# Kernel optimization log

Measured on AMD Instinct MI355X. Metric: run time of the kernel, lower is better.

The kernel has to match this reference:

```python
import jax, jax.numpy as jnp
import numpy as np

INF = 1e5
EPS = 1e-8
B, NRES, NRIG = 1, 448, 512
C_S, C_Z, C_H, H, PQ, PV = 384, 128, 16, 12, 4, 8


def _quat_to_rot(q):
    q = q / jnp.linalg.norm(q, axis=-1, keepdims=True)
    w, x, y, z = q[..., 0], q[..., 1], q[..., 2], q[..., 3]
    return jnp.stack([
        jnp.stack([1 - 2 * (y * y + z * z), 2 * (x * y - w * z), 2 * (x * z + w * y)], -1),
        jnp.stack([2 * (x * y + w * z), 1 - 2 * (x * x + z * z), 2 * (y * z - w * x)], -1),
        jnp.stack([2 * (x * z - w * y), 2 * (y * z + w * x), 1 - 2 * (x * x + y * y)], -1),
    ], -2)


def setup_inputs() -> dict:
    key = jax.random.key(0)
    ks = jax.random.split(key, 16)
    lin = lambda k, i, o: (jax.random.normal(k, (i, o), jnp.float32) / np.sqrt(i))
    hc = H * C_H
    return dict(
        s=jax.random.normal(ks[0], (B, NRIG, C_S), jnp.float32),
        z=jax.random.normal(ks[1], (B, NRES, NRES, C_Z), jnp.float32),
        rot=_quat_to_rot(jax.random.normal(ks[2], (B, NRIG, 4), jnp.float32)),
        trans=jax.random.normal(ks[3], (B, NRIG, 3), jnp.float32) * 10.0,
        mask=jnp.ones((B, NRIG), jnp.float32),
        rigid_to_res_idx=jax.random.randint(ks[4], (B, NRIG), 0, NRES),
        w_q=lin(ks[5], C_S, hc), b_q=jnp.zeros((hc,), jnp.float32),
        w_kv=lin(ks[6], C_S, 2 * hc), b_kv=jnp.zeros((2 * hc,), jnp.float32),
        w_qp=lin(ks[7], C_S, H * PQ * 3), b_qp=jnp.zeros((H * PQ * 3,), jnp.float32),
        w_kvp=lin(ks[8], C_S, H * (PQ + PV) * 3), b_kvp=jnp.zeros((H * (PQ + PV) * 3,), jnp.float32),
        w_b=lin(ks[9], C_Z, H), b_b=jnp.zeros((H,), jnp.float32),
        w_dz=lin(ks[10], C_Z, C_Z // 4), b_dz=jnp.zeros((C_Z // 4,), jnp.float32),
        head_weights=jnp.full((H,), 0.5413, jnp.float32),  # softplus^-1(1)
        w_out=lin(ks[11], H * (C_Z // 4 + C_H + PV * 4), C_S),
        b_out=jnp.zeros((C_S,), jnp.float32),
    )


def _fwd(s, z, rot, trans, mask, rigid_to_res_idx,
         w_q, b_q, w_kv, b_kv, w_qp, b_qp, w_kvp, b_kvp,
         w_b, b_b, w_dz, b_dz, head_weights, w_out, b_out):
    Bd, nr, _ = s.shape
    nres = z.shape[-2]
    h = w_b.shape[-1]
    ch = w_q.shape[-1] // h
    pq = w_qp.shape[-1] // (3 * h)
    pkv = w_kvp.shape[-1] // (3 * h)
    pv = pkv - pq

    q = (s @ w_q + b_q).reshape(Bd, nr, h, ch)
    kv = (s @ w_kv + b_kv).reshape(Bd, nr, h, 2 * ch)
    k, v = kv[..., :ch], kv[..., ch:]

    def to_pts(flat):
        # flat: [B,nr,3*D] laid out as 3 coordinate chunks -> global-frame pts [B,nr,D,3]
        D = flat.shape[-1] // 3
        p = jnp.moveaxis(flat.reshape(Bd, nr, 3, D), -2, -1)
        return jnp.einsum('bnij,bndj->bndi', rot, p) + trans[:, :, None, :]

    q_pts = to_pts(s @ w_qp + b_qp).reshape(Bd, nr, h, pq, 3)
    kv_pts = to_pts(s @ w_kvp + b_kvp).reshape(Bd, nr, h, pkv, 3)
    k_pts, v_pts = kv_pts[..., :pq, :], kv_pts[..., pq:, :]

    # pair bias gathered rigid->res on both axes
    bi = jnp.arange(Bd)[:, None, None]
    b_pair = z @ w_b + b_b  # [B,Nres,Nres,H]
    b_bcast = b_pair[bi, rigid_to_res_idx[:, :, None], rigid_to_res_idx[:, None, :]]  # [B,nr,nr,H]

    a = jnp.einsum('bihc,bjhc->bhij', q, k) * np.sqrt(1.0 / (3 * ch))
    a = a + np.sqrt(1.0 / 3) * jnp.moveaxis(b_bcast, -1, -3)

    # squared-distance point attention
    diff = q_pts[:, :, None] - k_pts[:, None]  # [B,nr,nr,h,pq,3]
    sq = jnp.sum(diff * diff, -1)              # [B,nr,nr,h,pq]
    hw = jax.nn.softplus(head_weights) * np.sqrt(1.0 / (3 * (pq * 9.0 / 2)))
    pt_att = -0.5 * jnp.sum(sq * hw[:, None], -1)  # [B,nr,nr,h]
    a = a + jnp.moveaxis(pt_att, -1, -3)

    sq_mask = INF * (mask[:, :, None] * mask[:, None, :] - 1.0)
    a = jax.nn.softmax(a + sq_mask[:, None], axis=-1)  # [B,h,nr,nr]

    o = jnp.einsum('bhij,bjhc->bihc', a, v).reshape(Bd, nr, h * ch)

    o_pt_g = jnp.einsum('bhij,bjhpx->bihpx', a, v_pts)  # [B,nr,h,pv,3]
    o_pt = jnp.einsum('bnji,bnhpj->bnhpi', rot, o_pt_g - trans[:, :, None, None, :])  # invert_apply
    o_pt_norm = jnp.sqrt(jnp.sum(o_pt * o_pt, -1) + EPS).reshape(Bd, nr, h * pv)
    o_pt = o_pt.reshape(Bd, nr, h * pv, 3)

    pair_z = z @ w_dz + b_dz  # [B,Nres,Nres,cz4]
    pz_rig = pair_z[jnp.arange(Bd)[:, None], rigid_to_res_idx]  # [B,nr,Nres,cz4]
    # faithful to the torch scatter_add_: the index varies over the QUERY rigid i
    # (constant over keys j), so row i's full softmax mass lands in column res(i).
    onehot = jax.nn.one_hot(rigid_to_res_idx, nres, dtype=a.dtype)  # [B,nr,Nres]
    a_agg = a.sum(-1)[..., None] * onehot[:, None]  # [B,h,nr,Nres]
    o_pair = jnp.einsum('bhin,bind->bihd', a_agg, pz_rig).reshape(Bd, nr, -1)

    feats = jnp.concatenate([o, o_pt[..., 0], o_pt[..., 1], o_pt[..., 2], o_pt_norm, o_pair], -1)
    return feats @ w_out + b_out


def reference(s, z, rot, trans, mask, rigid_to_res_idx, w_q, b_q, w_kv, b_kv, w_qp, b_qp, w_kvp, b_kvp, w_b, b_b, w_dz, b_dz, head_weights, w_out, b_out):
    return _fwd(s, z, rot, trans, mask, rigid_to_res_idx, w_q, b_q, w_kv, b_kv, w_qp, b_qp, w_kvp, b_kvp, w_b, b_b, w_dz, b_dz, head_weights, w_out, b_out)
```

## Files before the change

### kernel.cpp

```cpp
#include <hip/hip_runtime.h>
#include <hip/hip_bf16.h>
#include <math.h>

constexpr int NRIG = 512;
constexpr int NRES = 448;
constexpr int CS   = 384;
constexpr int CZ   = 128;
constexpr int CH   = 16;
constexpr int NH   = 12;
constexpr int PQ   = 4;
constexpr int PV   = 8;
constexpr int HC   = NH * CH;
constexpr float INF_ = 100000.0f;

constexpr size_t OFF_Q   = 0;
constexpr size_t OFF_K   = OFF_Q   + (size_t)NH*NRIG*16;
constexpr size_t OFF_QP  = OFF_K   + (size_t)NH*NRIG*16;
constexpr size_t OFF_KP  = OFF_QP  + (size_t)NH*NRIG*12;
constexpr size_t OFF_VT  = OFF_KP  + (size_t)NH*NRIG*12;
constexpr size_t OFF_PZ  = OFF_VT  + (size_t)NH*40*NRIG;
constexpr size_t OFF_O   = OFF_PZ  + (size_t)NRIG*32;
constexpr size_t OFF_OPT = OFF_O   + (size_t)NRIG*HC;
constexpr size_t OFF_RS  = OFF_OPT + (size_t)NRIG*NH*PV*3;
constexpr size_t OFF_B   = OFF_RS  + (size_t)NRIG*NH;
constexpr size_t OFF_RAW = OFF_B;
constexpr size_t OFF_F   = OFF_B;

__global__ __launch_bounds__(256) void proj_gemm_kernel(
    const float* __restrict__ s,
    const float* __restrict__ wq,  const float* __restrict__ bq,
    const float* __restrict__ wkv, const float* __restrict__ bkv,
    const float* __restrict__ wqp, const float* __restrict__ bqp,
    const float* __restrict__ wkvp,const float* __restrict__ bkvp,
    float* __restrict__ ws)
{
    constexpr int BM=64, BN=32, BK=32, LDA=68;
    __shared__ float sA[BK][LDA];
    __shared__ float sB[BK][BN];
    const int m0 = blockIdx.x * BM;
    const int c0 = blockIdx.y * BN;
    const int t  = threadIdx.x;
    const int tx = t & 15, ty = t >> 4;

    float acc[4][2] = {};

    for (int kt = 0; kt < CS/BK; ++kt) {
        const int k0 = kt*BK;
        #pragma unroll
        for (int r = 0; r < 2; ++r) {
            int qd = r*256 + t;
            int m = qd >> 3, kq = (qd & 7) << 2;
            float4 f = *(const float4*)(s + (size_t)(m0+m)*CS + k0 + kq);
            sA[kq+0][m] = f.x; sA[kq+1][m] = f.y;
            sA[kq+2][m] = f.z; sA[kq+3][m] = f.w;
        }
        {
            int kk = t >> 3, c4 = (t & 7) << 2;
            int c = c0 + c4;
            const float* wp; int ld, co;
            if (c < 192)      { wp = wq;   ld = 192; co = c;     }
            else if (c < 576) { wp = wkv;  ld = 384; co = c-192; }
            else if (c < 720) { wp = wqp;  ld = 144; co = c-576; }
            else              { wp = wkvp; ld = 432; co = c-720; }
            float4 f = *(const float4*)(wp + (size_t)(k0+kk)*ld + co);
            *(float4*)&sB[kk][c4] = f;
        }
        __syncthreads();
        #pragma unroll
        for (int kk = 0; kk < BK; ++kk) {
            float4 a = *(const float4*)&sA[kk][ty*4];
            float2 b = *(const float2*)&sB[kk][tx*2];
            acc[0][0] += a.x*b.x; acc[0][1] += a.x*b.y;
            acc[1][0] += a.y*b.x; acc[1][1] += a.y*b.y;
            acc[2][0] += a.z*b.x; acc[2][1] += a.z*b.y;
            acc[3][0] += a.w*b.x; acc[3][1] += a.w*b.y;
        }
        __syncthreads();
    }

    float* qw  = ws + OFF_Q;  float* kw = ws + OFF_K;  float* vt = ws + OFF_VT;
    float* raw = ws + OFF_RAW;
    #pragma unroll
    for (int i = 0; i < 4; ++i)
        #pragma unroll
        for (int j = 0; j < 2; ++j) {
            int n = m0 + ty*4 + i;
            int c = c0 + tx*2 + j;
            if (c < 192) {
                int hh = c >> 4, cc = c & 15;
                qw[((size_t)hh*NRIG + n)*16 + cc] = acc[i][j] + bq[c];
            } else if (c < 576) {
                int e = c-192; float val = acc[i][j] + bkv[e];
                int hh = e >> 5, sub = e & 31;
                if (sub < CH) kw[((size_t)hh*NRIG + n)*16 + sub] = val;
                else          vt[((size_t)hh*40 + (sub-CH))*NRIG + n] = val;
            } else {
                int e = c-576;
                float bb_ = (c < 720) ? bqp[e] : bkvp[c-720];
                raw[(size_t)n*576 + e] = acc[i][j] + bb_;
            }
        }
}

__global__ __launch_bounds__(256) void rotate_kernel(
    const float* __restrict__ rot, const float* __restrict__ trans,
    float* __restrict__ ws)
{
    const int gid = blockIdx.x*256 + threadIdx.x;
    const int n = gid / 192, d = gid % 192;
    const float* raw = ws + OFF_RAW + (size_t)n*576;
    float px, py, pzz;
    if (d < 48) { px = raw[d];      py = raw[48+d];       pzz = raw[96+d]; }
    else { int dd = d-48; px = raw[144+dd]; py = raw[288+dd]; pzz = raw[432+dd]; }
    const float* R = rot   + (size_t)n*9;
    const float* T = trans + (size_t)n*3;
    float gx = R[0]*px + R[1]*py + R[2]*pzz + T[0];
    float gy = R[3]*px + R[4]*py + R[5]*pzz + T[1];
    float gz = R[6]*px + R[7]*py + R[8]*pzz + T[2];
    if (d < 48) {
        int hh = d >> 2, pp = d & 3;
        float* dst = ws + OFF_QP + ((size_t)hh*NRIG + n)*12 + pp*3;
        dst[0]=gx; dst[1]=gy; dst[2]=gz;
    } else {
        int dd = d-48; int hh = dd/12, pp = dd%12;
        if (pp < PQ) {
            float* dst = ws + OFF_KP + ((size_t)hh*NRIG + n)*12 + pp*3;
            dst[0]=gx; dst[1]=gy; dst[2]=gz;
        } else {
            float* vt = ws + OFF_VT + ((size_t)hh*40 + 16 + (pp-PQ)*3)*NRIG + n;
            vt[0*NRIG]=gx; vt[1*NRIG]=gy; vt[2*NRIG]=gz;
        }
    }
}

__global__ __launch_bounds__(256) void bpair_kernel(
    const float* __restrict__ z, const int* __restrict__ ridx,
    const float* __restrict__ wb, const float* __restrict__ bb,
    const float* __restrict__ wdz, const float* __restrict__ bdz,
    float* __restrict__ ws)
{
    __shared__ float4 sWb[CZ*3];
    __shared__ float sZd[CZ];
    const int t = threadIdx.x;
    const int i = blockIdx.x;
    const int ri = ridx[i];
    for (int e = t; e < CZ*3; e += 256) sWb[e] = ((const float4*)wb)[e];
    if (t < CZ) sZd[t] = z[((size_t)ri*NRES + ri)*CZ + t];
    __syncthreads();

    const int j0  = t, j1 = t + 256;
    const int rj0 = ridx[j0], rj1 = ridx[j1];
    const float4* zr0 = (const float4*)(z + ((size_t)ri*NRES + rj0)*CZ);
    const float4* zr1 = (const float4*)(z + ((size_t)ri*NRES + rj1)*CZ);

    float a0[12], a1[12];
    #pragma unroll
    for (int hh=0; hh<12; ++hh) { a0[hh]=0.f; a1[hh]=0.f; }

    #pragma unroll 4
    for (int c4 = 0; c4 < 32; ++c4) {
        float4 z0 = zr0[c4], z1 = zr1[c4];
        #pragma unroll
        for (int e = 0; e < 4; ++e) {
            const int c = (c4<<2) + e;
            float wv[12];
            *(float4*)&wv[0] = sWb[c*3+0];
            *(float4*)&wv[4] = sWb[c*3+1];
            *(float4*)&wv[8] = sWb[c*3+2];
            const float zv0 = (&z0.x)[e];
            const float zv1 = (&z1.x)[e];
            #pragma unroll
            for (int hh=0; hh<12; ++hh) { a0[hh] += zv0*wv[hh]; a1[hh] += zv1*wv[hh]; }
        }
    }
    const float SC = 0.57735026918962584f;
    float* bbc = ws + OFF_B;
    #pragma unroll
    for (int hh = 0; hh < 12; ++hh) {
        float bias = bb[hh];
        bbc[((size_t)hh*NRIG + i)*NRIG + j0] = (a0[hh]+bias)*SC;
        bbc[((size_t)hh*NRIG + i)*NRIG + j1] = (a1[hh]+bias)*SC;
    }
    if (t < 32) {
        float acc = 0.f;
        for (int c = 0; c < CZ; ++c) acc += sZd[c] * wdz[(size_t)c*32 + t];
        (ws + OFF_PZ)[(size_t)i*32 + t] = acc + bdz[t];
    }
}

__global__ __launch_bounds__(256) void attn_kernel(
    const float* __restrict__ hw_in, const float* __restrict__ mask,
    float* __restrict__ ws)
{
    constexpr int TI = 4;
    const int h    = blockIdx.x;
    const int i0   = blockIdx.y * TI;
    const int t    = threadIdx.x;
    const int lane = t & 63, wid = t >> 6;

    __shared__ float sQ[TI][16];
    __shared__ float sQP[TI][12];
    __shared__ float sE[TI][512];
    __shared__ float redM[TI][4], redS[TI][4];
    __shared__ float sMi[TI];
    __shared__ float sP[TI][16][44];

    const float* qw  = ws + OFF_Q  + (size_t)h*NRIG*16;
    const float* kw  = ws + OFF_K  + (size_t)h*NRIG*16;
    const float* qpw = ws + OFF_QP + (size_t)h*NRIG*12;
    const float* kpw = ws + OFF_KP + (size_t)h*NRIG*12;
    const float* vt  = ws + OFF_VT + (size_t)h*40*NRIG;
    const float* bbc = ws + OFF_B  + (size_t)h*NRIG*NRIG;

    for (int e = t; e < TI*16; e += 256) sQ[e/16][e%16]  = qw[(size_t)(i0+e/16)*16 + (e%16)];
    for (int e = t; e < TI*12; e += 256) sQP[e/12][e%12] = qpw[(size_t)(i0+e/12)*12 + (e%12)];
    if (t < TI) sMi[t] = mask[i0+t];
    __syncthreads();

    const float hwv = -0.5f * log1pf(__expf(hw_in[h])) * 0.13608276348795434f;
    const float QKS = 0.14433756729740643f;

    float lg[2][TI];
    float lmax[TI] = {-1e30f,-1e30f,-1e30f,-1e30f};
    #pragma unroll
    for (int jj = 0; jj < 2; ++jj) {
        int j = t + jj*256;
        float kk[16], kpv[12];
        const float4* kr = (const float4*)(kw + (size_t)j*16);
        *(float4*)&kk[0]=kr[0]; *(float4*)&kk[4]=kr[1]; *(float4*)&kk[8]=kr[2]; *(float4*)&kk[12]=kr[3];
        const float4* kpr = (const float4*)(kpw + (size_t)j*12);
        *(float4*)&kpv[0]=kpr[0]; *(float4*)&kpv[4]=kpr[1]; *(float4*)&kpv[8]=kpr[2];
        float mj = mask[j];
        #pragma unroll
        for (int qq = 0; qq < TI; ++qq) {
            float dot = 0.f;
            #pragma unroll
            for (int c = 0; c < 16; ++c) dot += sQ[qq][c]*kk[c];
            float sq = 0.f;
            #pragma unroll
            for (int e = 0; e < 12; ++e) { float d = sQP[qq][e]-kpv[e]; sq += d*d; }
            float bv = bbc[(size_t)(i0+qq)*NRIG + j];
            float lgt = dot*QKS + bv + hwv*sq + INF_*(sMi[qq]*mj - 1.0f);
            lg[jj][qq] = lgt;
            lmax[qq] = fmaxf(lmax[qq], lgt);
        }
    }
    #pragma unroll
    for (int sft = 1; sft < 64; sft <<= 1)
        #pragma unroll
        for (int qq=0;qq<TI;++qq) lmax[qq] = fmaxf(lmax[qq], __shfl_xor(lmax[qq], sft));
    if (lane == 0) { for (int qq=0;qq<TI;++qq) redM[qq][wid] = lmax[qq]; }
    __syncthreads();
    float M[TI], psum[TI];
    #pragma unroll
    for (int qq=0;qq<TI;++qq) {
        M[qq] = fmaxf(fmaxf(redM[qq][0],redM[qq][1]),fmaxf(redM[qq][2],redM[qq][3]));
        psum[qq]=0.f;
    }
    #pragma unroll
    for (int jj = 0; jj < 2; ++jj) {
        int j = t + jj*256;
        #pragma unroll
        for (int qq=0;qq<TI;++qq) {
            float e = __expf(lg[jj][qq] - M[qq]);
            sE[qq][j] = e;
            psum[qq] += e;
        }
    }
    #pragma unroll
    for (int sft = 1; sft < 64; sft <<= 1)
        #pragma unroll
        for (int qq=0;qq<TI;++qq) psum[qq] += __shfl_xor(psum[qq], sft);
    if (lane == 0) { for (int qq=0;qq<TI;++qq) redS[qq][wid] = psum[qq]; }
    __syncthreads();

    {
        const int c0 = wid*10;
        float acc[10][TI];
        #pragma unroll
        for (int ci=0;ci<10;++ci)
            #pragma unroll
            for (int qq=0;qq<TI;++qq) acc[ci][qq]=0.f;

        #pragma unroll
        for (int m = 0; m < 8; ++m) {
            const int j = lane + 64*m;
            float ev[TI];
            #pragma unroll
            for (int qq=0;qq<TI;++qq) ev[qq] = sE[qq][j];
            #pragma unroll
            for (int ci = 0; ci < 10; ++ci) {
                float vv = vt[(size_t)(c0+ci)*NRIG + j];
                #pragma unroll
                for (int qq=0;qq<TI;++qq) acc[ci][qq] += ev[qq]*vv;
            }
        }
        #pragma unroll
        for (int ci=0;ci<10;++ci)
            #pragma unroll
            for (int qq=0;qq<TI;++qq) {
                acc[ci][qq] += __shfl_xor(acc[ci][qq], 1);
                acc[ci][qq] += __shfl_xor(acc[ci][qq], 2);
            }
        if ((lane & 3) == 0) {
            const int g = lane >> 2;
            #pragma unroll
            for (int qq=0;qq<TI;++qq)
                #pragma unroll
                for (int ci=0;ci<10;++ci)
                    sP[qq][g][c0+ci] = acc[ci][qq];
        }
    }
    __syncthreads();

    if (t < TI*41) {
        const int qq = t / 41, c = t % 41;
        const int n = i0 + qq;
        float S = redS[qq][0]+redS[qq][1]+redS[qq][2]+redS[qq][3];
        float Sinv = 1.0f / S;
        if (c == 40) {
            (ws + OFF_RS)[(size_t)n*NH + h] = S * Sinv;
        } else {
            float acc = 0.f;
            #pragma unroll
            for (int g = 0; g < 16; ++g) acc += sP[qq][g][c];
            acc *= Sinv;
            if (c < 16) (ws + OFF_O  )[((size_t)n*NH + h)*CH + c]      = acc;
            else        (ws + OFF_OPT)[((size_t)n*NH + h)*24 + (c-16)] = acc;
        }
    }
}

__global__ __launch_bounds__(256) void feats_kernel(
    const float* __restrict__ rot, const float* __restrict__ trans,
    float* __restrict__ ws)
{
    constexpr int TI = 4;
    const int i0 = blockIdx.x*TI;
    const int t  = threadIdx.x;
    float* F = ws + OFF_F;
    const float* o_ws = ws + OFF_O;  const float* optg = ws + OFF_OPT;
    const float* rs   = ws + OFF_RS; const float* pz   = ws + OFF_PZ;

    for (int e = t; e < TI*HC; e += 256) {
        int qq = e/HC, c = e%HC;
        F[(size_t)(i0+qq)*960 + c] = o_ws[(size_t)(i0+qq)*HC + c];
    }
    for (int e = t; e < TI*96; e += 256) {
        int qq = e/96, hp = e%96; int n = i0+qq;
        const float* g = optg + ((size_t)n*NH + hp/PV)*24 + (hp%PV)*3;
        float gx = g[0]-trans[n*3+0], gy = g[1]-trans[n*3+1], gz = g[2]-trans[n*3+2];
        const float* R = rot + (size_t)n*9;
        float lx = R[0]*gx + R[3]*gy + R[6]*gz;
        float ly = R[1]*gx + R[4]*gy + R[7]*gz;
        float lz = R[2]*gx + R[5]*gy + R[8]*gz;
        float* Fr = F + (size_t)n*960;
        Fr[192+hp] = lx; Fr[288+hp] = ly; Fr[384+hp] = lz;
        Fr[480+hp] = sqrtf(lx*lx+ly*ly+lz*lz + 1e-8f);
    }
    for (int e = t; e < TI*384; e += 256) {
        int qq = e/384, hd = e%384; int n = i0+qq;
        F[(size_t)n*960 + 576 + hd] = rs[(size_t)n*NH + hd/32] * pz[(size_t)n*32 + (hd%32)];
    }
}

__global__ __launch_bounds__(256) void out_gemm_kernel(
    const float* __restrict__ w_out, const float* __restrict__ b_out,
    const float* __restrict__ ws, float* __restrict__ out)
{
    constexpr int BM=64, BN=32, BK=32, LDA=68;
    __shared__ float sA[BK][LDA];
    __shared__ float sB[BK][BN];
    const float* F = ws + OFF_F;
    const int m0 = blockIdx.x * BM;
    const int c0 = blockIdx.y * BN;
    const int t  = threadIdx.x;
    const int tx = t & 15, ty = t >> 4;

    float acc[4][2] = {};

    for (int kt = 0; kt < 960/BK; ++kt) {
        const int k0 = kt*BK;
        #pragma unroll
        for (int r = 0; r < 2; ++r) {
            int qd = r*256 + t;
            int m = qd >> 3, kq = (qd & 7) << 2;
            float4 f = *(const float4*)(F + (size_t)(m0+m)*960 + k0 + kq);
            sA[kq+0][m] = f.x; sA[kq+1][m] = f.y;
            sA[kq+2][m] = f.z; sA[kq+3][m] = f.w;
        }
        {
            int kk = t >> 3, c4 = (t & 7) << 2;
            float4 f = *(const float4*)(w_out + (size_t)(k0+kk)*CS + c0 + c4);
            *(float4*)&sB[kk][c4] = f;
        }
        __syncthreads();
        #pragma unroll
        for (int kk = 0; kk < BK; ++kk) {
            float4 a = *(const float4*)&sA[kk][ty*4];
            float2 b = *(const float2*)&sB[kk][tx*2];
            acc[0][0] += a.x*b.x; acc[0][1] += a.x*b.y;
            acc[1][0] += a.y*b.x; acc[1][1] += a.y*b.y;
            acc[2][0] += a.z*b.x; acc[2][1] += a.z*b.y;
            acc[3][0] += a.w*b.x; acc[3][1] += a.w*b.y;
        }
        __syncthreads();
    }

    #pragma unroll
    for (int i = 0; i < 4; ++i)
        #pragma unroll
        for (int j = 0; j < 2; ++j) {
            int n = m0 + ty*4 + i;
            int c = c0 + tx*2 + j;
            out[(size_t)n*CS + c] = acc[i][j] + b_out[c];
        }
}

extern "C" void kernel_launch(void* const* d_in, const int* in_sizes, int n_in,
                              void* d_out, int out_size, void* d_ws, size_t ws_size,
                              hipStream_t stream)
{
    const float* s     = (const float*)d_in[0];
    const float* z     = (const float*)d_in[1];
    const float* rot   = (const float*)d_in[2];
    const float* trans = (const float*)d_in[3];
    const float* mask  = (const float*)d_in[4];
    const int*   ridx  = (const int*)  d_in[5];
    const float* wq    = (const float*)d_in[6];
    const float* bq    = (const float*)d_in[7];
    const float* wkv   = (const float*)d_in[8];
    const float* bkv   = (const float*)d_in[9];
    const float* wqp   = (const float*)d_in[10];
    const float* bqp   = (const float*)d_in[11];
    const float* wkvp  = (const float*)d_in[12];
    const float* bkvp  = (const float*)d_in[13];
    const float* wb    = (const float*)d_in[14];
    const float* bb    = (const float*)d_in[15];
    const float* wdz   = (const float*)d_in[16];
    const float* bdz   = (const float*)d_in[17];
    const float* hw    = (const float*)d_in[18];
    const float* wout  = (const float*)d_in[19];
    const float* bout  = (const float*)d_in[20];
    float* ws  = (float*)d_ws;
    float* out = (float*)d_out;

    hipLaunchKernelGGL(proj_gemm_kernel, dim3(NRIG/64, 1152/32), dim3(256), 0, stream,
        s, wq,bq, wkv,bkv, wqp,bqp, wkvp,bkvp, ws);
    hipLaunchKernelGGL(rotate_kernel, dim3(NRIG*192/256), dim3(256), 0, stream,
        rot, trans, ws);
    hipLaunchKernelGGL(bpair_kernel, dim3(NRIG), dim3(256), 0, stream,
        z, ridx, wb, bb, wdz, bdz, ws);
    hipLaunchKernelGGL(attn_kernel, dim3(NH, NRIG/4), dim3(256), 0, stream,
        hw, mask, ws);
    hipLaunchKernelGGL(feats_kernel, dim3(NRIG/4), dim3(256), 0, stream,
        rot, trans, ws);
    hipLaunchKernelGGL(out_gemm_kernel, dim3(NRIG/64, CS/32), dim3(256), 0, stream,
        wout, bout, ws, out);
}
```

Measured before the change: 122.0 us.

## Compute pair bias over all residue pairs, gather in attention, transpose K layouts

The pair-bias projection now runs once over every residue pair of z, writing a compact [Nres*Nres,12] table. The attention kernel gathers from this table by rigid-to-residue index instead of reading a precomputed per-head [H,Nrig,Nrig] bias. The diagonal z row used for pair_z moves into the feats kernel. K and K-point tensors are stored transposed so per-key loads coalesce, and the output GEMM uses smaller tiles to launch more blocks. The full z is now read densely (about 100MB) rather than through gathered rows, and the attention bias loads become scattered gathers.

```diff
diff --git a/kernel.cpp b/kernel.cpp
--- a/kernel.cpp
+++ b/kernel.cpp
@@ -11,20 +11,20 @@
 constexpr int PQ   = 4;
 constexpr int PV   = 8;
 constexpr int HC   = NH * CH;
+constexpr int NPAIR = NRES*NRES;
 constexpr float INF_ = 100000.0f;
 
 constexpr size_t OFF_Q   = 0;
-constexpr size_t OFF_K   = OFF_Q   + (size_t)NH*NRIG*16;
-constexpr size_t OFF_QP  = OFF_K   + (size_t)NH*NRIG*16;
-constexpr size_t OFF_KP  = OFF_QP  + (size_t)NH*NRIG*12;
-constexpr size_t OFF_VT  = OFF_KP  + (size_t)NH*NRIG*12;
-constexpr size_t OFF_PZ  = OFF_VT  + (size_t)NH*40*NRIG;
-constexpr size_t OFF_O   = OFF_PZ  + (size_t)NRIG*32;
+constexpr size_t OFF_KT  = OFF_Q   + (size_t)NH*NRIG*16;
+constexpr size_t OFF_QP  = OFF_KT  + (size_t)NH*16*NRIG;
+constexpr size_t OFF_KPT = OFF_QP  + (size_t)NH*NRIG*12;
+constexpr size_t OFF_VT  = OFF_KPT + (size_t)NH*12*NRIG;
+constexpr size_t OFF_O   = OFF_VT  + (size_t)NH*40*NRIG;
 constexpr size_t OFF_OPT = OFF_O   + (size_t)NRIG*HC;
 constexpr size_t OFF_RS  = OFF_OPT + (size_t)NRIG*NH*PV*3;
-constexpr size_t OFF_B   = OFF_RS  + (size_t)NRIG*NH;
-constexpr size_t OFF_RAW = OFF_B;
-constexpr size_t OFF_F   = OFF_B;
+constexpr size_t OFF_BP  = OFF_RS  + (size_t)NRIG*NH;
+constexpr size_t OFF_RAW = OFF_BP;
+constexpr size_t OFF_F   = OFF_BP;
 
 __global__ __launch_bounds__(256) void proj_gemm_kernel(
     const float* __restrict__ s,
@@ -78,7 +78,7 @@
         __syncthreads();
     }
 
-    float* qw  = ws + OFF_Q;  float* kw = ws + OFF_K;  float* vt = ws + OFF_VT;
+    float* qw  = ws + OFF_Q;  float* ktw = ws + OFF_KT;  float* vt = ws + OFF_VT;
     float* raw = ws + OFF_RAW;
     #pragma unroll
     for (int i = 0; i < 4; ++i)
@@ -92,8 +92,8 @@
             } else if (c < 576) {
                 int e = c-192; float val = acc[i][j] + bkv[e];
                 int hh = e >> 5, sub = e & 31;
-                if (sub < CH) kw[((size_t)hh*NRIG + n)*16 + sub] = val;
-                else          vt[((size_t)hh*40 + (sub-CH))*NRIG + n] = val;
+                if (sub < CH) ktw[((size_t)hh*16 + sub)*NRIG + n] = val;
+                else          vt [((size_t)hh*40 + (sub-CH))*NRIG + n] = val;
             } else {
                 int e = c-576;
                 float bb_ = (c < 720) ? bqp[e] : bkvp[c-720];
@@ -124,8 +124,10 @@
     } else {
         int dd = d-48; int hh = dd/12, pp = dd%12;
         if (pp < PQ) {
-            float* dst = ws + OFF_KP + ((size_t)hh*NRIG + n)*12 + pp*3;
-            dst[0]=gx; dst[1]=gy; dst[2]=gz;
+            float* kpt = ws + OFF_KPT + (size_t)hh*12*NRIG;
+            kpt[(size_t)(pp*3+0)*NRIG + n] = gx;
+            kpt[(size_t)(pp*3+1)*NRIG + n] = gy;
+            kpt[(size_t)(pp*3+2)*NRIG + n] = gz;
         } else {
             float* vt = ws + OFF_VT + ((size_t)hh*40 + 16 + (pp-PQ)*3)*NRIG + n;
             vt[0*NRIG]=gx; vt[1*NRIG]=gy; vt[2*NRIG]=gz;
@@ -133,63 +135,45 @@
     }
 }
 
-__global__ __launch_bounds__(256) void bpair_kernel(
-    const float* __restrict__ z, const int* __restrict__ ridx,
+__global__ __launch_bounds__(256) void zwb_kernel(
+    const float* __restrict__ z,
     const float* __restrict__ wb, const float* __restrict__ bb,
-    const float* __restrict__ wdz, const float* __restrict__ bdz,
     float* __restrict__ ws)
 {
-    __shared__ float4 sWb[CZ*3];
-    __shared__ float sZd[CZ];
+    constexpr int BR = 64, LDZ = 132;
+    __shared__ float sZ[BR][LDZ];
+    __shared__ float sW[CZ*12];
     const int t = threadIdx.x;
-    const int i = blockIdx.x;
-    const int ri = ridx[i];
-    for (int e = t; e < CZ*3; e += 256) sWb[e] = ((const float4*)wb)[e];
-    if (t < CZ) sZd[t] = z[((size_t)ri*NRES + ri)*CZ + t];
-    __syncthreads();
-
-    const int j0  = t, j1 = t + 256;
-    const int rj0 = ridx[j0], rj1 = ridx[j1];
-    const float4* zr0 = (const float4*)(z + ((size_t)ri*NRES + rj0)*CZ);
-    const float4* zr1 = (const float4*)(z + ((size_t)ri*NRES + rj1)*CZ);
-
-    float a0[12], a1[12];
-    #pragma unroll
-    for (int hh=0; hh<12; ++hh) { a0[hh]=0.f; a1[hh]=0.f; }
-
-    #pragma unroll 4
-    for (int c4 = 0; c4 < 32; ++c4) {
-        float4 z0 = zr0[c4], z1 = zr1[c4];
-        #pragma unroll
-        for (int e = 0; e < 4; ++e) {
-            const int c = (c4<<2) + e;
-            float wv[12];
-            *(float4*)&wv[0] = sWb[c*3+0];
-            *(float4*)&wv[4] = sWb[c*3+1];
-            *(float4*)&wv[8] = sWb[c*3+2];
-            const float zv0 = (&z0.x)[e];
-            const float zv1 = (&z1.x)[e];
-            #pragma unroll
-            for (int hh=0; hh<12; ++hh) { a0[hh] += zv0*wv[hh]; a1[hh] += zv1*wv[hh]; }
-        }
+    const size_t r0 = (size_t)blockIdx.x * BR;
+
+    for (int e = t; e < CZ*12; e += 256) sW[e] = wb[e];
+    #pragma unroll
+    for (int p = 0; p < 8; ++p) {
+        int q = p*256 + t;
+        int r = q >> 5, c4 = (q & 31) << 2;
+        float4 f = *(const float4*)(z + (r0 + r)*CZ + c4);
+        *(float4*)&sZ[r][c4] = f;
+    }
+    __syncthreads();
+
+    const int r = t >> 2, g = t & 3;
+    float a0=0.f, a1=0.f, a2=0.f;
+    #pragma unroll 8
+    for (int c = 0; c < CZ; ++c) {
+        float zv = sZ[r][c];
+        const float* w = &sW[c*12 + g*3];
+        a0 += zv*w[0]; a1 += zv*w[1]; a2 += zv*w[2];
     }
     const float SC = 0.57735026918962584f;
-    float* bbc = ws + OFF_B;
-    #pragma unroll
-    for (int hh = 0; hh < 12; ++hh) {
-        float bias = bb[hh];
-        bbc[((size_t)hh*NRIG + i)*NRIG + j0] = (a0[hh]+bias)*SC;
-        bbc[((size_t)hh*NRIG + i)*NRIG + j1] = (a1[hh]+bias)*SC;
-    }
-    if (t < 32) {
-        float acc = 0.f;
-        for (int c = 0; c < CZ; ++c) acc += sZd[c] * wdz[(size_t)c*32 + t];
-        (ws + OFF_PZ)[(size_t)i*32 + t] = acc + bdz[t];
-    }
+    float* bp = ws + OFF_BP + (r0 + r)*12 + g*3;
+    bp[0] = (a0 + bb[g*3+0])*SC;
+    bp[1] = (a1 + bb[g*3+1])*SC;
+    bp[2] = (a2 + bb[g*3+2])*SC;
 }
 
 __global__ __launch_bounds__(256) void attn_kernel(
     const float* __restrict__ hw_in, const float* __restrict__ mask,
+    const int* __restrict__ ridx,
     float* __restrict__ ws)
 {
     constexpr int TI = 4;
@@ -203,18 +187,19 @@
     __shared__ float sE[TI][512];
     __shared__ float redM[TI][4], redS[TI][4];
     __shared__ float sMi[TI];
+    __shared__ int   sRi[TI];
     __shared__ float sP[TI][16][44];
 
-    const float* qw  = ws + OFF_Q  + (size_t)h*NRIG*16;
-    const float* kw  = ws + OFF_K  + (size_t)h*NRIG*16;
-    const float* qpw = ws + OFF_QP + (size_t)h*NRIG*12;
-    const float* kpw = ws + OFF_KP + (size_t)h*NRIG*12;
-    const float* vt  = ws + OFF_VT + (size_t)h*40*NRIG;
-    const float* bbc = ws + OFF_B  + (size_t)h*NRIG*NRIG;
+    const float* qw  = ws + OFF_Q   + (size_t)h*NRIG*16;
+    const float* ktw = ws + OFF_KT  + (size_t)h*16*NRIG;
+    const float* qpw = ws + OFF_QP  + (size_t)h*NRIG*12;
+    const float* kpt = ws + OFF_KPT + (size_t)h*12*NRIG;
+    const float* vt  = ws + OFF_VT  + (size_t)h*40*NRIG;
+    const float* bp  = ws + OFF_BP;
 
     for (int e = t; e < TI*16; e += 256) sQ[e/16][e%16]  = qw[(size_t)(i0+e/16)*16 + (e%16)];
     for (int e = t; e < TI*12; e += 256) sQP[e/12][e%12] = qpw[(size_t)(i0+e/12)*12 + (e%12)];
-    if (t < TI) sMi[t] = mask[i0+t];
+    if (t < TI) { sMi[t] = mask[i0+t]; sRi[t] = ridx[i0+t]; }
     __syncthreads();
 
     const float hwv = -0.5f * log1pf(__expf(hw_in[h])) * 0.13608276348795434f;
@@ -226,11 +211,12 @@
     for (int jj = 0; jj < 2; ++jj) {
         int j = t + jj*256;
         float kk[16], kpv[12];
-        const float4* kr = (const float4*)(kw + (size_t)j*16);
-        *(float4*)&kk[0]=kr[0]; *(float4*)&kk[4]=kr[1]; *(float4*)&kk[8]=kr[2]; *(float4*)&kk[12]=kr[3];
-        const float4* kpr = (const float4*)(kpw + (size_t)j*12);
-        *(float4*)&kpv[0]=kpr[0]; *(float4*)&kpv[4]=kpr[1]; *(float4*)&kpv[8]=kpr[2];
+        #pragma unroll
+        for (int c = 0; c < 16; ++c) kk[c]  = ktw[(size_t)c*NRIG + j];
+        #pragma unroll
+        for (int e = 0; e < 12; ++e) kpv[e] = kpt[(size_t)e*NRIG + j];
         float mj = mask[j];
+        int rj = ridx[j];
         #pragma unroll
         for (int qq = 0; qq < TI; ++qq) {
             float dot = 0.f;
@@ -239,7 +225,7 @@
             float sq = 0.f;
             #pragma unroll
             for (int e = 0; e < 12; ++e) { float d = sQP[qq][e]-kpv[e]; sq += d*d; }
-            float bv = bbc[(size_t)(i0+qq)*NRIG + j];
+            float bv = bp[((size_t)sRi[qq]*NRES + rj)*12 + h];
             float lgt = dot*QKS + bv + hwv*sq + INF_*(sMi[qq]*mj - 1.0f);
             lg[jj][qq] = lgt;
             lmax[qq] = fmaxf(lmax[qq], lgt);
@@ -333,15 +319,24 @@
 
 __global__ __launch_bounds__(256) void feats_kernel(
     const float* __restrict__ rot, const float* __restrict__ trans,
+    const float* __restrict__ z, const int* __restrict__ ridx,
+    const float* __restrict__ wdz, const float* __restrict__ bdz,
     float* __restrict__ ws)
 {
     constexpr int TI = 4;
+    __shared__ float sZd[TI][CZ];
+    __shared__ float sPz[TI][32];
     const int i0 = blockIdx.x*TI;
     const int t  = threadIdx.x;
     float* F = ws + OFF_F;
     const float* o_ws = ws + OFF_O;  const float* optg = ws + OFF_OPT;
-    const float* rs   = ws + OFF_RS; const float* pz   = ws + OFF_PZ;
-
+    const float* rs   = ws + OFF_RS;
+
+    for (int e = t; e < TI*CZ; e += 256) {
+        int qq = e >> 7, c = e & 127;
+        int ri = ridx[i0+qq];
+        sZd[qq][c] = z[((size_t)ri*NRES + ri)*CZ + c];
+    }
     for (int e = t; e < TI*HC; e += 256) {
         int qq = e/HC, c = e%HC;
         F[(size_t)(i0+qq)*960 + c] = o_ws[(size_t)(i0+qq)*HC + c];
@@ -358,9 +353,18 @@
         Fr[192+hp] = lx; Fr[288+hp] = ly; Fr[384+hp] = lz;
         Fr[480+hp] = sqrtf(lx*lx+ly*ly+lz*lz + 1e-8f);
     }
+    __syncthreads();
+    if (t < TI*32) {
+        int qq = t >> 5, d = t & 31;
+        float acc = 0.f;
+        #pragma unroll 8
+        for (int c = 0; c < CZ; ++c) acc += sZd[qq][c] * wdz[(size_t)c*32 + d];
+        sPz[qq][d] = acc + bdz[d];
+    }
+    __syncthreads();
     for (int e = t; e < TI*384; e += 256) {
         int qq = e/384, hd = e%384; int n = i0+qq;
-        F[(size_t)n*960 + 576 + hd] = rs[(size_t)n*NH + hd/32] * pz[(size_t)n*32 + (hd%32)];
+        F[(size_t)n*960 + 576 + hd] = rs[(size_t)n*NH + (hd>>5)] * sPz[qq][hd&31];
     }
 }
 
@@ -368,7 +372,7 @@
     const float* __restrict__ w_out, const float* __restrict__ b_out,
     const float* __restrict__ ws, float* __restrict__ out)
 {
-    constexpr int BM=64, BN=32, BK=32, LDA=68;
+    constexpr int BM=32, BN=16, BK=32, LDA=36;
     __shared__ float sA[BK][LDA];
     __shared__ float sB[BK][BN];
     const float* F = ws + OFF_F;
@@ -377,44 +381,35 @@
     const int t  = threadIdx.x;
     const int tx = t & 15, ty = t >> 4;
 
-    float acc[4][2] = {};
+    float acc0 = 0.f, acc1 = 0.f;
 
     for (int kt = 0; kt < 960/BK; ++kt) {
         const int k0 = kt*BK;
-        #pragma unroll
-        for (int r = 0; r < 2; ++r) {
-            int qd = r*256 + t;
-            int m = qd >> 3, kq = (qd & 7) << 2;
+        {
+            int m = t >> 3, kq = (t & 7) << 2;
             float4 f = *(const float4*)(F + (size_t)(m0+m)*960 + k0 + kq);
             sA[kq+0][m] = f.x; sA[kq+1][m] = f.y;
             sA[kq+2][m] = f.z; sA[kq+3][m] = f.w;
         }
-        {
-            int kk = t >> 3, c4 = (t & 7) << 2;
+        if (t < 128) {
+            int kk = t >> 2, c4 = (t & 3) << 2;
             float4 f = *(const float4*)(w_out + (size_t)(k0+kk)*CS + c0 + c4);
             *(float4*)&sB[kk][c4] = f;
         }
         __syncthreads();
         #pragma unroll
         for (int kk = 0; kk < BK; ++kk) {
-            float4 a = *(const float4*)&sA[kk][ty*4];
-            float2 b = *(const float2*)&sB[kk][tx*2];
-            acc[0][0] += a.x*b.x; acc[0][1] += a.x*b.y;
-            acc[1][0] += a.y*b.x; acc[1][1] += a.y*b.y;
-            acc[2][0] += a.z*b.x; acc[2][1] += a.z*b.y;
-            acc[3][0] += a.w*b.x; acc[3][1] += a.w*b.y;
+            float b  = sB[kk][tx];
+            acc0 += sA[kk][ty*2+0]*b;
+            acc1 += sA[kk][ty*2+1]*b;
         }
         __syncthreads();
     }
 
-    #pragma unroll
-    for (int i = 0; i < 4; ++i)
-        #pragma unroll
-        for (int j = 0; j < 2; ++j) {
-            int n = m0 + ty*4 + i;
-            int c = c0 + tx*2 + j;
-            out[(size_t)n*CS + c] = acc[i][j] + b_out[c];
-        }
+    const int c = c0 + tx;
+    const float bv = b_out[c];
+    out[(size_t)(m0 + ty*2+0)*CS + c] = acc0 + bv;
+    out[(size_t)(m0 + ty*2+1)*CS + c] = acc1 + bv;
 }
 
 extern "C" void kernel_launch(void* const* d_in, const int* in_sizes, int n_in,
@@ -449,12 +444,12 @@
         s, wq,bq, wkv,bkv, wqp,bqp, wkvp,bkvp, ws);
     hipLaunchKernelGGL(rotate_kernel, dim3(NRIG*192/256), dim3(256), 0, stream,
         rot, trans, ws);
-    hipLaunchKernelGGL(bpair_kernel, dim3(NRIG), dim3(256), 0, stream,
-        z, ridx, wb, bb, wdz, bdz, ws);
+    hipLaunchKernelGGL(zwb_kernel, dim3(NPAIR/64), dim3(256), 0, stream,
+        z, wb, bb, ws);
     hipLaunchKernelGGL(attn_kernel, dim3(NH, NRIG/4), dim3(256), 0, stream,
-        hw, mask, ws);
+        hw, mask, ridx, ws);
     hipLaunchKernelGGL(feats_kernel, dim3(NRIG/4), dim3(256), 0, stream,
-        rot, trans, ws);
-    hipLaunchKernelGGL(out_gemm_kernel, dim3(NRIG/64, CS/32), dim3(256), 0, stream,
+        rot, trans, z, ridx, wdz, bdz, ws);
+    hipLaunchKernelGGL(out_gemm_kernel, dim3(NRIG/32, CS/16), dim3(256), 0, stream,
         wout, bout, ws, out);
 }
```

Measured after the change: 133.8 us. +9.7%, slower.
